# Optimization experiments

Measured on AMD Instinct MI355X. Metric: run time of the kernel, lower is better.

## Reference

```python
import jax, jax.numpy as jnp
import numpy as np

HEADS = 16
DIMS = [64, 64, 64, 64]  # [d_att(Q), d_att(K), d_ff(V), d_ff(G)]
EPS = 1e-4
P_POW = 2


def _cdist(Q, K):
    # Euclidean pairwise distance via the norm expansion, like torch.cdist.
    # Q: [h, b, t, d], K: [h, b, t, d] -> [h, b, t, t]
    q2 = jnp.sum(Q * Q, axis=-1)  # [h, b, t]
    k2 = jnp.sum(K * K, axis=-1)  # [h, b, t]
    qk = jnp.einsum('hbtd,hbsd->hbts', Q, K)
    d2 = q2[..., :, None] + k2[..., None, :] - 2.0 * qk
    return jnp.sqrt(jnp.maximum(d2, 0.0))


def setup_inputs() -> dict:
    key = jax.random.key(0)
    ks = jax.random.split(key, 4)
    b, t, d_in = 2, 2048, 1024
    d_proj = HEADS * sum(DIMS)  # 4096
    X = jax.random.normal(ks[0], (b, t, d_in), dtype=jnp.float32)
    W_in = jax.random.normal(ks[1], (d_in, d_proj), dtype=jnp.float32) * (d_in ** -0.5)
    b_in = jnp.zeros((d_proj,), dtype=jnp.float32)
    W_out = jax.random.normal(ks[2], (HEADS * DIMS[2], d_in), dtype=jnp.float32) * ((HEADS * DIMS[2]) ** -0.5)
    b_out = jnp.zeros((d_in,), dtype=jnp.float32)
    return {"X": X, "W_in": W_in, "b_in": b_in, "W_out": W_out, "b_out": b_out}


def reference(X, W_in, b_in, W_out, b_out):
    b, t, _ = X.shape
    # multi-head input projection: [b,t,d_in] -> [h,b,t,sum(DIMS)] -> split
    P = X @ W_in + b_in                       # [b, t, h*sum(DIMS)]
    P = P.reshape(b, t, HEADS, sum(DIMS))
    P = jnp.transpose(P, (2, 0, 1, 3))        # [h, b, t, sum(DIMS)]
    splits = np.cumsum(DIMS)[:-1]
    Q, K, V, G = jnp.split(P, splits, axis=-1)
    # Shepard's attention: inverse-power-distance weights
    W = jnp.power(EPS + _cdist(Q, K), -P_POW)         # [h, b, t, t]
    W = W / (EPS + jnp.sum(W, axis=-1, keepdims=True))
    A = jnp.einsum('hbts,hbse->hbte', W, V)           # [h, b, t, e]
    H = G * A                                          # gating
    H = jnp.transpose(H, (1, 2, 0, 3)).reshape(b, t, HEADS * DIMS[2])
    return H @ W_out + b_out
```

## Files before the change

kernel.cpp:

```cpp
#include <hip/hip_runtime.h>
#include <hip/hip_bf16.h>
#include <cstdint>
#include <cstddef>

typedef __bf16 bf16_t;
typedef __attribute__((ext_vector_type(8))) __bf16 bf16x8;
typedef __attribute__((ext_vector_type(4))) __bf16 bf16x4;
typedef __attribute__((ext_vector_type(4))) float f32x4;
typedef __attribute__((ext_vector_type(4))) unsigned int u32x4;

#define ATT_EPS 1e-4f

__device__ __forceinline__ f32x4 mfma_bf16(bf16x8 a, bf16x8 b, f32x4 c) {
  return __builtin_amdgcn_mfma_f32_16x16x32_bf16(a, b, c, 0, 0, 0);
}

#define GLDS16(g, l)                                                          \
  __builtin_amdgcn_global_load_lds(                                           \
      (const __attribute__((address_space(1))) void*)(g),                     \
      (__attribute__((address_space(3))) void*)(l), 16, 0, 0)

__global__ __launch_bounds__(256) void cvt_x_kernel(
    const float* __restrict__ X, bf16_t* __restrict__ Xb, int n8) {
  int i = blockIdx.x * 256 + threadIdx.x;
  if (i >= n8) return;
  f32x4 a = ((const f32x4*)X)[i * 2 + 0];
  f32x4 b = ((const f32x4*)X)[i * 2 + 1];
  bf16x8 o;
  o[0] = (__bf16)a[0]; o[1] = (__bf16)a[1]; o[2] = (__bf16)a[2]; o[3] = (__bf16)a[3];
  o[4] = (__bf16)b[0]; o[5] = (__bf16)b[1]; o[6] = (__bf16)b[2]; o[7] = (__bf16)b[3];
  ((bf16x8*)Xb)[i] = o;
}

__global__ __launch_bounds__(256) void tcvt_kernel(
    const float* __restrict__ W, bf16_t* __restrict__ Wt, int R, int C) {
  __shared__ float T[64][65];
  int tx = threadIdx.x & 63, ty = threadIdx.x >> 6;
  int c0 = blockIdx.x * 64, r0 = blockIdx.y * 64;
#pragma unroll
  for (int i = 0; i < 16; ++i) {
    int rr = ty * 16 + i;
    T[rr][tx] = W[(size_t)(r0 + rr) * C + c0 + tx];
  }
  __syncthreads();
#pragma unroll
  for (int i = 0; i < 16; ++i) {
    int cc = ty * 16 + i;
    Wt[(size_t)(c0 + cc) * R + r0 + tx] = (bf16_t)T[tx][cc];
  }
}

__global__ __launch_bounds__(256) void vt_kernel(
    const bf16_t* __restrict__ P, bf16_t* __restrict__ VtG) {
  __shared__ float T[64][65];
  int h = blockIdx.x;
  int r0 = blockIdx.y * 64;
  int tx = threadIdx.x & 63, ty = threadIdx.x >> 6;
  const bf16_t* src = P + (size_t)r0 * 4096 + h * 256 + 128;
#pragma unroll
  for (int i = 0; i < 16; ++i) {
    int rr = ty * 16 + i;
    T[rr][tx] = (float)src[(size_t)rr * 4096 + tx];
  }
  __syncthreads();
#pragma unroll
  for (int i = 0; i < 16; ++i) {
    int cc = ty * 16 + i;
    VtG[(size_t)(h * 64 + cc) * 4096 + r0 + tx] = (bf16_t)T[tx][cc];
  }
}

template <int OUTF32>
__global__ __launch_bounds__(256, 2) void gemm_kernel(
    const bf16_t* __restrict__ A, const bf16_t* __restrict__ Bt,
    const float* __restrict__ bias, void* __restrict__ Cout,
    int M, int N, int K) {
  __shared__ bf16_t As[2][128 * 64];
  __shared__ bf16_t Bs[2][128 * 64];
  int tid = threadIdx.x, lane = tid & 63, wv = tid >> 6;
  int l15 = lane & 15, lhi = lane >> 4;
  int NT = N >> 7;
  int nwg = gridDim.x;
  int qq = nwg >> 3;
  int swz = (blockIdx.x & 7) * qq + (blockIdx.x >> 3);
  int tm = swz / NT, tn = swz % NT;
  int m0 = tm << 7, n0 = tn << 7;
  int wm = (wv >> 1) << 6, wn = (wv & 1) << 6;
  int KT = K >> 6;

  auto stage = [&](int buf, int kt) {
    int k0 = kt << 6;
#pragma unroll
    for (int s = 0; s < 4; ++s) {
      int t = s * 256 + tid;
      int row = t >> 3, u = t & 7;
      int cc = (u ^ (row & 7)) << 3;
      GLDS16(A + (size_t)(m0 + row) * K + k0 + cc, &As[buf][t * 8]);
    }
#pragma unroll
    for (int s = 0; s < 4; ++s) {
      int t = s * 256 + tid;
      int row = t >> 3, u = t & 7;
      int cc = (u ^ (row & 7)) << 3;
      GLDS16(Bt + (size_t)(n0 + row) * K + k0 + cc, &Bs[buf][t * 8]);
    }
  };

  f32x4 zero = {0.f, 0.f, 0.f, 0.f};
  f32x4 acc[4][4];
#pragma unroll
  for (int ms = 0; ms < 4; ++ms)
#pragma unroll
    for (int ns = 0; ns < 4; ++ns) acc[ms][ns] = zero;

  stage(0, 0);
  __syncthreads();
  int cur = 0;
  for (int kt = 0; kt < KT; ++kt) {
    if (kt + 1 < KT) stage(cur ^ 1, kt + 1);
#pragma unroll
    for (int ks = 0; ks < 2; ++ks) {
      bf16x8 af[4], bfr[4];
#pragma unroll
      for (int ms = 0; ms < 4; ++ms) {
        int row = wm + ms * 16 + l15;
        af[ms] = *(const bf16x8*)&As[cur][row * 64 + (((ks * 4 + lhi) ^ (row & 7)) << 3)];
      }
#pragma unroll
      for (int ns = 0; ns < 4; ++ns) {
        int col = wn + ns * 16 + l15;
        bfr[ns] = *(const bf16x8*)&Bs[cur][col * 64 + (((ks * 4 + lhi) ^ (col & 7)) << 3)];
      }
#pragma unroll
      for (int ms = 0; ms < 4; ++ms)
#pragma unroll
        for (int ns = 0; ns < 4; ++ns)
          acc[ms][ns] = mfma_bf16(af[ms], bfr[ns], acc[ms][ns]);
    }
    __syncthreads();
    cur ^= 1;
  }

#pragma unroll
  for (int ns = 0; ns < 4; ++ns) {
    int col = n0 + wn + ns * 16 + l15;
    float bv = bias[col];
#pragma unroll
    for (int ms = 0; ms < 4; ++ms) {
      int rowb = m0 + wm + ms * 16 + lhi * 4;
#pragma unroll
      for (int r = 0; r < 4; ++r) {
        float v = acc[ms][ns][r] + bv;
        if (OUTF32)
          ((float*)Cout)[(size_t)(rowb + r) * N + col] = v;
        else
          ((bf16_t*)Cout)[(size_t)(rowb + r) * N + col] = (bf16_t)v;
      }
    }
  }
}

__global__ __launch_bounds__(256) void norms_kernel(
    const bf16_t* __restrict__ P, float* __restrict__ Q2, float* __restrict__ K2) {
  int tid = threadIdx.x, lane = tid & 63, wv = tid >> 6;
  int wg = blockIdx.x * 4 + wv;
  int h = wg >> 9, rb = wg & 511;
  int r = rb * 8 + (lane >> 3), ch = lane & 7;
  const bf16_t* base = P + (size_t)r * 4096 + h * 256 + ch * 8;
  bf16x8 qv = *(const bf16x8*)base;
  bf16x8 kv = *(const bf16x8*)(base + 64);
  float sq = 0.f, sk = 0.f;
#pragma unroll
  for (int j = 0; j < 8; ++j) {
    float a = (float)qv[j];
    sq += a * a;
    float c = (float)kv[j];
    sk += c * c;
  }
#pragma unroll
  for (int m = 1; m <= 4; m <<= 1) {
    sq += __shfl_xor(sq, m);
    sk += __shfl_xor(sk, m);
  }
  if (ch == 0) {
    Q2[h * 4096 + r] = sq;
    K2[h * 4096 + r] = sk;
  }
}

__global__ __launch_bounds__(256, 2) void attn_kernel(
    const bf16_t* __restrict__ P, const bf16_t* __restrict__ VtG,
    const float* __restrict__ Q2, const float* __restrict__ K2,
    bf16_t* __restrict__ H) {
  __shared__ bf16_t Ks[128 * 64];
  __shared__ bf16_t Vts[64 * 128];
  __shared__ bf16_t Wb[4][32 * 136];

  int tid = threadIdx.x, lane = tid & 63, wv = tid >> 6;
  int l15 = lane & 15, lhi = lane >> 4;
  int swz = (blockIdx.x & 7) * 64 + (blockIdx.x >> 3);
  int hb = swz >> 4, qt = swz & 15;
  int h = hb >> 1, b = hb & 1;
  int rowbase = b * 2048;
  const bf16_t* Pq = P + (size_t)rowbase * 4096 + h * 256;
  const bf16_t* Pk = Pq + 64;
  const bf16_t* Pg = Pq + 192;
  const bf16_t* Vg = VtG + (size_t)h * 64 * 4096 + rowbase;
  const float* Q2g = Q2 + h * 4096 + rowbase;
  const float* K2g = K2 + h * 4096 + rowbase;
  int q0 = qt * 128 + wv * 32;

  bf16x8 qm[2][2];
#pragma unroll
  for (int qs = 0; qs < 2; ++qs)
#pragma unroll
    for (int ks = 0; ks < 2; ++ks) {
      int row = q0 + qs * 16 + l15;
      bf16x8 q = *(const bf16x8*)(Pq + (size_t)row * 4096 + ks * 32 + lhi * 8);
      u32x4 u = *(u32x4*)&q;
      u = (u ^ 0x80008000u) + 0x00800080u;
      qm[qs][ks] = *(bf16x8*)&u;
    }
  float q2v[2];
#pragma unroll
  for (int qs = 0; qs < 2; ++qs) q2v[qs] = Q2g[q0 + qs * 16 + l15];

  f32x4 nacc[2][4];
  float dacc[2] = {0.f, 0.f};
#pragma unroll
  for (int qs = 0; qs < 2; ++qs)
#pragma unroll
    for (int es = 0; es < 4; ++es) nacc[qs][es] = (f32x4){0.f, 0.f, 0.f, 0.f};

  bf16_t* wbuf = &Wb[wv][0];

  for (int st = 0; st < 16; ++st) {
    int s0 = st * 128;
    __syncthreads();
#pragma unroll
    for (int s4 = 0; s4 < 4; ++s4) {
      int t = s4 * 256 + tid;
      int row = t >> 3, u = t & 7;
      int cc = (u ^ (row & 7)) << 3;
      GLDS16(Pk + (size_t)(s0 + row) * 4096 + cc, &Ks[t * 8]);
    }
#pragma unroll
    for (int s4 = 0; s4 < 4; ++s4) {
      int t = s4 * 256 + tid;
      int row = t >> 4, u = t & 15;
      int cc = (u ^ (row & 7)) << 3;
      GLDS16(Vg + (size_t)row * 4096 + s0 + cc, &Vts[t * 8]);
    }
    __syncthreads();

#pragma unroll
    for (int ss = 0; ss < 8; ++ss) {
      int srow = ss * 16 + l15;
      bf16x8 kf0 = *(const bf16x8*)&Ks[srow * 64 + ((lhi ^ (srow & 7)) << 3)];
      bf16x8 kf1 = *(const bf16x8*)&Ks[srow * 64 + (((4 + lhi) ^ (srow & 7)) << 3)];
      f32x4 k2v = *(const f32x4*)(K2g + s0 + ss * 16 + lhi * 4);
#pragma unroll
      for (int qs = 0; qs < 2; ++qs) {
        f32x4 S = mfma_bf16(kf0, qm[qs][0], k2v);
        S = mfma_bf16(kf1, qm[qs][1], S);
        bf16x4 wv4;
#pragma unroll
        for (int r = 0; r < 4; ++r) {
          float d2 = S[r] + q2v[qs];
          float w = __builtin_amdgcn_rcpf(fmaxf(d2, 1e-12f));
          dacc[qs] += w;
          wv4[r] = (__bf16)w;
        }
        *(bf16x4*)&wbuf[(qs * 16 + l15) * 136 + ss * 16 + lhi * 4] = wv4;
      }
    }
#pragma unroll
    for (int sk = 0; sk < 4; ++sk) {
      bf16x8 wf[2], vf[4];
#pragma unroll
      for (int qs = 0; qs < 2; ++qs)
        wf[qs] = *(const bf16x8*)&wbuf[(qs * 16 + l15) * 136 + sk * 32 + lhi * 8];
#pragma unroll
      for (int es = 0; es < 4; ++es) {
        int row = es * 16 + l15;
        vf[es] = *(const bf16x8*)&Vts[row * 128 + (((sk * 4 + lhi) ^ (row & 7)) << 3)];
      }
#pragma unroll
      for (int qs = 0; qs < 2; ++qs)
#pragma unroll
        for (int es = 0; es < 4; ++es)
          nacc[qs][es] = mfma_bf16(wf[qs], vf[es], nacc[qs][es]);
    }
  }

#pragma unroll
  for (int qs = 0; qs < 2; ++qs) {
    dacc[qs] += __shfl_xor(dacc[qs], 16);
    dacc[qs] += __shfl_xor(dacc[qs], 32);
  }

#pragma unroll
  for (int qs = 0; qs < 2; ++qs)
#pragma unroll
    for (int r = 0; r < 4; ++r) {
      int tq = q0 + qs * 16 + lhi * 4 + r;
      float dn = __shfl(dacc[qs], lhi * 4 + r);
      float inv = __builtin_amdgcn_rcpf(ATT_EPS + dn);
#pragma unroll
      for (int es = 0; es < 4; ++es) {
        int ec = es * 16 + l15;
        float g = (float)Pg[(size_t)tq * 4096 + ec];
        float hv = g * nacc[qs][es][r] * inv;
        H[(size_t)(rowbase + tq) * 1024 + h * 64 + ec] = (bf16_t)hv;
      }
    }
}

extern "C" void kernel_launch(void* const* d_in, const int* in_sizes, int n_in,
                              void* d_out, int out_size, void* d_ws, size_t ws_size,
                              hipStream_t stream) {
  const float* X     = (const float*)d_in[0];
  const float* W_in  = (const float*)d_in[1];
  const float* b_in  = (const float*)d_in[2];
  const float* W_out = (const float*)d_in[3];
  const float* b_out = (const float*)d_in[4];

  char* ws = (char*)d_ws;
  bf16_t* Xb  = (bf16_t*)(ws);
  bf16_t* VtG = (bf16_t*)(ws);
  bf16_t* WbT = (bf16_t*)(ws + ((size_t)8  << 20));
  bf16_t* WoT = (bf16_t*)(ws + ((size_t)16 << 20));
  bf16_t* Pb  = (bf16_t*)(ws + ((size_t)18 << 20));
  bf16_t* Hb  = (bf16_t*)(ws + ((size_t)50 << 20));
  float*  Q2  = (float*) (ws + ((size_t)58 << 20));
  float*  K2  = (float*) (ws + ((size_t)59 << 20));

  cvt_x_kernel<<<2048, 256, 0, stream>>>(X, Xb, 4096 * 1024 / 8);
  tcvt_kernel<<<dim3(64, 16), 256, 0, stream>>>(W_in, WbT, 1024, 4096);
  tcvt_kernel<<<dim3(16, 16), 256, 0, stream>>>(W_out, WoT, 1024, 1024);
  gemm_kernel<0><<<1024, 256, 0, stream>>>(Xb, WbT, b_in, Pb, 4096, 4096, 1024);
  norms_kernel<<<2048, 256, 0, stream>>>(Pb, Q2, K2);
  vt_kernel<<<dim3(16, 64), 256, 0, stream>>>(Pb, VtG);
  attn_kernel<<<512, 256, 0, stream>>>(Pb, VtG, Q2, K2, Hb);
  gemm_kernel<1><<<256, 256, 0, stream>>>(Hb, WoT, b_out, d_out, 4096, 1024, 1024);
}
```

Measured before the change: 143.3 us.

## Switch attention to 32x32x16 MFMA and keep weights in registers

Rewrites the attention inner loop around 32x32x16 bf16 MFMA tiles. The distance-weight tile now goes from the score accumulator straight into the A operand of the PV MFMA through packed bf16 converts and cross-half lane shuffles, which removes the per-wave LDS staging buffer for weights. It also frees LDS and raises the occupancy hint from 2 to 3 blocks per CU. The normalizer is passed through a small LDS array, synchronized only by an s_waitcnt with no barrier, which risks a race and adds register pressure.

Result: slower. 157.9 us (+10.2%).

```diff
diff --git a/kernel.cpp b/kernel.cpp
--- a/kernel.cpp
+++ b/kernel.cpp
@@ -7,12 +7,21 @@
 typedef __attribute__((ext_vector_type(8))) __bf16 bf16x8;
 typedef __attribute__((ext_vector_type(4))) __bf16 bf16x4;
 typedef __attribute__((ext_vector_type(4))) float f32x4;
+typedef __attribute__((ext_vector_type(16))) float f32x16;
 typedef __attribute__((ext_vector_type(4))) unsigned int u32x4;
 
 #define ATT_EPS 1e-4f
 
 __device__ __forceinline__ f32x4 mfma_bf16(bf16x8 a, bf16x8 b, f32x4 c) {
   return __builtin_amdgcn_mfma_f32_16x16x32_bf16(a, b, c, 0, 0, 0);
+}
+__device__ __forceinline__ f32x16 mfma32(bf16x8 a, bf16x8 b, f32x16 c) {
+  return __builtin_amdgcn_mfma_f32_32x32x16_bf16(a, b, c, 0, 0, 0);
+}
+__device__ __forceinline__ unsigned cvtpk_bf16(float lo, float hi) {
+  unsigned r;
+  asm("v_cvt_pk_bf16_f32 %0, %1, %2" : "=v"(r) : "v"(lo), "v"(hi));
+  return r;
 }
 
 #define GLDS16(g, l)                                                          \
@@ -188,16 +197,17 @@
   }
 }
 
-__global__ __launch_bounds__(256, 2) void attn_kernel(
+__global__ __launch_bounds__(256, 3) void attn_kernel(
     const bf16_t* __restrict__ P, const bf16_t* __restrict__ VtG,
     const float* __restrict__ Q2, const float* __restrict__ K2,
     bf16_t* __restrict__ H) {
   __shared__ bf16_t Ks[128 * 64];
   __shared__ bf16_t Vts[64 * 128];
-  __shared__ bf16_t Wb[4][32 * 136];
+  __shared__ float invLds[4][32];
 
   int tid = threadIdx.x, lane = tid & 63, wv = tid >> 6;
-  int l15 = lane & 15, lhi = lane >> 4;
+  int l31 = lane & 31, hi = lane >> 5, hi4 = hi * 4;
+  bool hiSel = (hi != 0);
   int swz = (blockIdx.x & 7) * 64 + (blockIdx.x >> 3);
   int hb = swz >> 4, qt = swz & 15;
   int h = hb >> 1, b = hb & 1;
@@ -210,29 +220,20 @@
   const float* K2g = K2 + h * 4096 + rowbase;
   int q0 = qt * 128 + wv * 32;
 
-  bf16x8 qm[2][2];
-#pragma unroll
-  for (int qs = 0; qs < 2; ++qs)
-#pragma unroll
-    for (int ks = 0; ks < 2; ++ks) {
-      int row = q0 + qs * 16 + l15;
-      bf16x8 q = *(const bf16x8*)(Pq + (size_t)row * 4096 + ks * 32 + lhi * 8);
-      u32x4 u = *(u32x4*)&q;
-      u = (u ^ 0x80008000u) + 0x00800080u;
-      qm[qs][ks] = *(bf16x8*)&u;
-    }
-  float q2v[2];
-#pragma unroll
-  for (int qs = 0; qs < 2; ++qs) q2v[qs] = Q2g[q0 + qs * 16 + l15];
-
-  f32x4 nacc[2][4];
-  float dacc[2] = {0.f, 0.f};
-#pragma unroll
-  for (int qs = 0; qs < 2; ++qs)
-#pragma unroll
-    for (int es = 0; es < 4; ++es) nacc[qs][es] = (f32x4){0.f, 0.f, 0.f, 0.f};
-
-  bf16_t* wbuf = &Wb[wv][0];
+  bf16x8 qm[4];
+#pragma unroll
+  for (int db = 0; db < 4; ++db) {
+    bf16x8 q = *(const bf16x8*)(Pq + (size_t)(q0 + l31) * 4096 + db * 16 + hi * 8);
+    u32x4 u = *(u32x4*)&q;
+    u = (u ^ 0x80008000u) + 0x00800080u;
+    qm[db] = *(bf16x8*)&u;
+  }
+  float q2s = Q2g[q0 + l31];
+
+  f32x16 nacc0, nacc1;
+#pragma unroll
+  for (int r = 0; r < 16; ++r) { nacc0[r] = 0.f; nacc1[r] = 0.f; }
+  float dacc0 = 0.f, dacc1 = 0.f;
 
   for (int st = 0; st < 16; ++st) {
     int s0 = st * 128;
@@ -253,67 +254,74 @@
     }
     __syncthreads();
 
-#pragma unroll
-    for (int ss = 0; ss < 8; ++ss) {
-      int srow = ss * 16 + l15;
-      bf16x8 kf0 = *(const bf16x8*)&Ks[srow * 64 + ((lhi ^ (srow & 7)) << 3)];
-      bf16x8 kf1 = *(const bf16x8*)&Ks[srow * 64 + (((4 + lhi) ^ (srow & 7)) << 3)];
-      f32x4 k2v = *(const f32x4*)(K2g + s0 + ss * 16 + lhi * 4);
-#pragma unroll
-      for (int qs = 0; qs < 2; ++qs) {
-        f32x4 S = mfma_bf16(kf0, qm[qs][0], k2v);
-        S = mfma_bf16(kf1, qm[qs][1], S);
-        bf16x4 wv4;
-#pragma unroll
-        for (int r = 0; r < 4; ++r) {
-          float d2 = S[r] + q2v[qs];
-          float w = __builtin_amdgcn_rcpf(fmaxf(d2, 1e-12f));
-          dacc[qs] += w;
-          wv4[r] = (__bf16)w;
-        }
-        *(bf16x4*)&wbuf[(qs * 16 + l15) * 136 + ss * 16 + lhi * 4] = wv4;
-      }
-    }
-#pragma unroll
-    for (int sk = 0; sk < 4; ++sk) {
-      bf16x8 wf[2], vf[4];
-#pragma unroll
-      for (int qs = 0; qs < 2; ++qs)
-        wf[qs] = *(const bf16x8*)&wbuf[(qs * 16 + l15) * 136 + sk * 32 + lhi * 8];
-#pragma unroll
-      for (int es = 0; es < 4; ++es) {
-        int row = es * 16 + l15;
-        vf[es] = *(const bf16x8*)&Vts[row * 128 + (((sk * 4 + lhi) ^ (row & 7)) << 3)];
-      }
-#pragma unroll
-      for (int qs = 0; qs < 2; ++qs)
-#pragma unroll
-        for (int es = 0; es < 4; ++es)
-          nacc[qs][es] = mfma_bf16(wf[qs], vf[es], nacc[qs][es]);
-    }
-  }
-
-#pragma unroll
-  for (int qs = 0; qs < 2; ++qs) {
-    dacc[qs] += __shfl_xor(dacc[qs], 16);
-    dacc[qs] += __shfl_xor(dacc[qs], 32);
-  }
-
-#pragma unroll
-  for (int qs = 0; qs < 2; ++qs)
-#pragma unroll
-    for (int r = 0; r < 4; ++r) {
-      int tq = q0 + qs * 16 + lhi * 4 + r;
-      float dn = __shfl(dacc[qs], lhi * 4 + r);
-      float inv = __builtin_amdgcn_rcpf(ATT_EPS + dn);
-#pragma unroll
-      for (int es = 0; es < 4; ++es) {
-        int ec = es * 16 + l15;
-        float g = (float)Pg[(size_t)tq * 4096 + ec];
-        float hv = g * nacc[qs][es][r] * inv;
-        H[(size_t)(rowbase + tq) * 1024 + h * 64 + ec] = (bf16_t)hv;
-      }
-    }
+    const float* K2t = K2g + s0;
+#pragma unroll
+    for (int sb = 0; sb < 4; ++sb) {
+      f32x16 D;
+#pragma unroll
+      for (int g = 0; g < 4; ++g) {
+        f32x4 k2v = *(const f32x4*)(K2t + sb * 32 + g * 8 + hi4);
+#pragma unroll
+        for (int j = 0; j < 4; ++j) D[g * 4 + j] = k2v[j] + q2s;
+      }
+#pragma unroll
+      for (int db = 0; db < 4; ++db) {
+        int srow = sb * 32 + l31;
+        bf16x8 kf = *(const bf16x8*)&Ks[srow * 64 + (((db * 2 + hi) ^ (srow & 7)) << 3)];
+        D = mfma32(kf, qm[db], D);
+      }
+      float p[16];
+#pragma unroll
+      for (int r = 0; r < 16; ++r) {
+        float w = __builtin_amdgcn_rcpf(fmaxf(D[r], 1e-12f));
+        if (r & 1) dacc1 += w; else dacc0 += w;
+        p[r] = w;
+      }
+      unsigned t01 = cvtpk_bf16(p[0], p[1]),  t23 = cvtpk_bf16(p[2], p[3]);
+      unsigned t45 = cvtpk_bf16(p[4], p[5]),  t67 = cvtpk_bf16(p[6], p[7]);
+      unsigned t89 = cvtpk_bf16(p[8], p[9]),  tab = cvtpk_bf16(p[10], p[11]);
+      unsigned tcd = cvtpk_bf16(p[12], p[13]), tef = cvtpk_bf16(p[14], p[15]);
+      unsigned x01 = __shfl_xor(t01, 32), x23 = __shfl_xor(t23, 32);
+      unsigned x45 = __shfl_xor(t45, 32), x67 = __shfl_xor(t67, 32);
+      unsigned x89 = __shfl_xor(t89, 32), xab = __shfl_xor(tab, 32);
+      unsigned xcd = __shfl_xor(tcd, 32), xef = __shfl_xor(tef, 32);
+      u32x4 w0v = {hiSel ? x45 : t01, hiSel ? x67 : t23,
+                   hiSel ? t45 : x01, hiSel ? t67 : x23};
+      u32x4 w1v = {hiSel ? xcd : t89, hiSel ? xef : tab,
+                   hiSel ? tcd : x89, hiSel ? tef : xab};
+      bf16x8 pa0 = *(bf16x8*)&w0v;
+      bf16x8 pa1 = *(bf16x8*)&w1v;
+      int e = l31;
+      {
+        int c0 = ((sb * 4 + 0 + hi) ^ (e & 7)) << 3;
+        int c1 = ((sb * 4 + 2 + hi) ^ (e & 7)) << 3;
+        bf16x8 vb00 = *(const bf16x8*)&Vts[e * 128 + c0];
+        bf16x8 vb01 = *(const bf16x8*)&Vts[(e + 32) * 128 + (((sb * 4 + 0 + hi) ^ ((e + 32) & 7)) << 3)];
+        bf16x8 vb10 = *(const bf16x8*)&Vts[e * 128 + c1];
+        bf16x8 vb11 = *(const bf16x8*)&Vts[(e + 32) * 128 + (((sb * 4 + 2 + hi) ^ ((e + 32) & 7)) << 3)];
+        nacc0 = mfma32(pa0, vb00, nacc0);
+        nacc1 = mfma32(pa0, vb01, nacc1);
+        nacc0 = mfma32(pa1, vb10, nacc0);
+        nacc1 = mfma32(pa1, vb11, nacc1);
+      }
+    }
+  }
+
+  float dacc = dacc0 + dacc1;
+  dacc += __shfl_xor(dacc, 32);
+  float inv = __builtin_amdgcn_rcpf(ATT_EPS + dacc);
+  if (lane < 32) invLds[wv][l31] = inv;
+  __builtin_amdgcn_s_waitcnt(0);
+#pragma unroll
+  for (int r = 0; r < 16; ++r) {
+    int q = (r & 3) + 8 * (r >> 2) + hi4;
+    int tq = q0 + q;
+    float iv = invLds[wv][q];
+    float g0 = (float)Pg[(size_t)tq * 4096 + l31];
+    float g1 = (float)Pg[(size_t)tq * 4096 + 32 + l31];
+    H[(size_t)(rowbase + tq) * 1024 + h * 64 + l31] = (bf16_t)(g0 * nacc0[r] * iv);
+    H[(size_t)(rowbase + tq) * 1024 + h * 64 + 32 + l31] = (bf16_t)(g1 * nacc1[r] * iv);
+  }
 }
 
 extern "C" void kernel_launch(void* const* d_in, const int* in_sizes, int n_in,
```
